# Performance work log

Measured on AMD Instinct MI355X. Metric: run time of the kernel, lower is better.

The kernel has to match this reference:

```python
import jax, jax.numpy as jnp
import numpy as np

DECAY = 0.9


def setup_inputs() -> dict:
    key = jax.random.key(0)
    k1, k2, k3 = jax.random.split(key, 3)
    B, S, D, M = 4, 4096, 1024, 4096
    x = jax.random.normal(k1, (B, S, D), dtype=jnp.float32)
    w1 = jax.random.normal(k2, (M, D), dtype=jnp.float32) * (1.0 / np.sqrt(D))
    w2 = jax.random.normal(k3, (D, M), dtype=jnp.float32) * (1.0 / np.sqrt(M))
    return {"x": x, "w1": w1, "w2": w2}


def reference(x, w1, w2):
    B, S, D = x.shape
    idx = jnp.arange(S)
    diff = idx[:, None] - idx[None, :]          # [S, S]
    mask = diff >= 0
    # clamp negative exponents before pow to avoid inf, then mask
    d = jnp.where(mask, diff, 0).astype(x.dtype)
    decay_matrix = (DECAY ** d) * (1.0 - DECAY) * mask.astype(x.dtype)  # [S, S]
    # causal exponential-decay EMA as dense matmul: current[b,t] = sum_s dm[t,s] x[b,s]
    current_states = jnp.einsum('ts,bsd->btd', decay_matrix, x)
    # roll by 1 with zeroed first step
    previous_states = jnp.concatenate(
        [jnp.zeros_like(current_states[:, :1]), current_states[:, :-1]], axis=1)
    # MemoryMLP: w2(silu(w1(prev)))
    h = jax.nn.silu(jnp.einsum('btd,md->btm', previous_states, w1))
    mem_out = jnp.einsum('btm,dm->btd', h, w2)
    final_state = current_states[:, -1, :]
    surprise_loss = jnp.mean((mem_out - jax.lax.stop_gradient(x)) ** 2)
    return mem_out, surprise_loss, final_state
```

## Files before the change

### kernel.cpp

```cpp
#include <hip/hip_runtime.h>
#include <hip/hip_bf16.h>
#include <stdint.h>

#define BSZ 4
#define SEQ 4096
#define DIM 1024
#define MDIM 4096
#define DECAYF 0.9f
#define OMD 0.1f
#define CHUNK 128
#define NCHUNK 32
#define DECAY_CHUNK 1.3901844577868923e-06f

typedef __bf16 bf16_t;
typedef __bf16 bf16x8 __attribute__((ext_vector_type(8)));
typedef __bf16 bf16x4 __attribute__((ext_vector_type(4)));
typedef float floatx4 __attribute__((ext_vector_type(4)));

__device__ __forceinline__ void load16_lds(const void* g, void* l) {
  __builtin_amdgcn_global_load_lds(
      (__attribute__((address_space(1))) void*)g,
      (__attribute__((address_space(3))) void*)l,
      16, 0, 0);
}

#define SB()  __builtin_amdgcn_sched_barrier(0)
#define BAR() __builtin_amdgcn_s_barrier()

__global__ void scan_chunk_kernel(const float* __restrict__ x,
                                  float* __restrict__ chunk_end) {
  int t = blockIdx.x * 256 + threadIdx.x;
  int d = t & (DIM - 1);
  int c = (t >> 10) & (NCHUNK - 1);
  int b = t >> 15;
  const float* xp = x + ((size_t)(b * SEQ + c * CHUNK + 64)) * DIM + d;
  float p = 0.f;
#pragma unroll 8
  for (int s = 0; s < 64; ++s) p = DECAYF * p + OMD * xp[(size_t)s * DIM];
  chunk_end[t] = p;
}

__global__ void scan_carry_kernel(const float* __restrict__ chunk_end,
                                  float* __restrict__ carry_in,
                                  float* __restrict__ final_state) {
  int t = blockIdx.x * 256 + threadIdx.x;
  int d = t & (DIM - 1);
  int b = t >> 10;
  float carry = 0.f;
#pragma unroll
  for (int c = 0; c < NCHUNK; ++c) {
    int idx = (b * NCHUNK + c) * DIM + d;
    carry_in[idx] = carry;
    carry = carry * DECAY_CHUNK + chunk_end[idx];
  }
  final_state[t] = carry;
}

__global__ void scan_emit_kernel(const float* __restrict__ x,
                                 const float* __restrict__ carry_in,
                                 bf16_t* __restrict__ prev) {
  int t = blockIdx.x * 256 + threadIdx.x;
  int d = t & (DIM - 1);
  int c = (t >> 10) & (NCHUNK - 1);
  int b = t >> 15;
  size_t base = ((size_t)(b * SEQ + c * CHUNK)) * DIM + d;
  const float* xp = x + base;
  bf16_t* pp = prev + base;
  float cs = carry_in[t];
#pragma unroll 4
  for (int s = 0; s < CHUNK; ++s) {
    pp[(size_t)s * DIM] = (bf16_t)cs;
    cs = DECAYF * cs + OMD * xp[(size_t)s * DIM];
  }
}

__global__ void cvt_bf16_kernel(const float* __restrict__ w, bf16_t* __restrict__ o) {
  int t = blockIdx.x * 256 + threadIdx.x;
  float4 v = ((const float4*)w)[t];
  bf16x4 r = { (bf16_t)v.x, (bf16_t)v.y, (bf16_t)v.z, (bf16_t)v.w };
  ((bf16x4*)o)[t] = r;
}

#define READ_A(dst, CA, MH)                                                    \
  _Pragma("unroll") for (int i_ = 0; i_ < 4; ++i_)                             \
      _Pragma("unroll") for (int k_ = 0; k_ < 2; ++k_)                         \
          dst[i_][k_] = *(const bf16x8*)((const char*)(CA) + wrBase +          \
                                         (MH) * 8192 + i_ * 2048 + rbase +     \
                                         ((k_ * 64 + kc) ^ lswz));

#define READ_B(dst, CB, NH)                                                    \
  _Pragma("unroll") for (int j_ = 0; j_ < 2; ++j_)                             \
      _Pragma("unroll") for (int k_ = 0; k_ < 2; ++k_)                         \
          dst[j_][k_] = *(const bf16x8*)((const char*)(CB) + wcBase +          \
                                         (NH) * 4096 + j_ * 2048 + rbase +     \
                                         ((k_ * 64 + kc) ^ lswz));

#define MMQ(AF, BF, MO, NO)                                                    \
  _Pragma("unroll") for (int k_ = 0; k_ < 2; ++k_)                             \
      _Pragma("unroll") for (int i_ = 0; i_ < 4; ++i_)                         \
          _Pragma("unroll") for (int j_ = 0; j_ < 2; ++j_)                     \
              acc[(MO) + i_][(NO) + j_] =                                      \
                  __builtin_amdgcn_mfma_f32_16x16x32_bf16(                     \
                      AF[i_][k_], BF[j_][k_], acc[(MO) + i_][(NO) + j_],       \
                      0, 0, 0);

template <int N, int K, int MT, int EPI>
__global__ __launch_bounds__(512, 1) void gemm256_kernel(
    const bf16_t* __restrict__ A, const bf16_t* __restrict__ B,
    void* __restrict__ Cout, const float* __restrict__ X,
    float* __restrict__ loss_acc) {
  constexpr int NT = N / 256;
  constexpr int NTK = K / 64;
  static_assert((NTK & 1) == 0 && NTK >= 4, "even K-tile count");
  static_assert(MT % 8 == 0, "m-tiles divisible by XCD count");
  __shared__ __attribute__((aligned(16))) bf16_t sA[2][16384];
  __shared__ __attribute__((aligned(16))) bf16_t sB[2][16384];

  const int tid = threadIdx.x;
  const int wave = tid >> 6;
  const int lane = tid & 63;
  const int bid = blockIdx.x;
  const int xcd = bid & 7;
  const int slot = bid >> 3;
  const int tm = (xcd * (MT / 8) + slot / NT) * 256;
  const int tn = (slot % NT) * 256;
  const int wr = wave >> 2;
  const int wc = wave & 3;
  const int wrBase = wr * 16384;
  const int wcBase = wc * 8192;
  const int rbase = (lane & 15) * 128;
  const int kc = (lane >> 4) * 16;
  const int lswz = ((lane >> 1) & 7) << 4;
  const int srow = wave * 8 + (lane >> 3);
  const int scolb = ((lane & 7) * 16) ^ (((srow >> 1) & 7) << 4);

  floatx4 acc[8][4];
#pragma unroll
  for (int i = 0; i < 8; ++i)
#pragma unroll
    for (int j = 0; j < 4; ++j) acc[i][j] = (floatx4){0.f, 0.f, 0.f, 0.f};

  bf16x8 a0[4][2], a1[4][2], b0[2][2], b1[2][2];

  auto stage_ht = [&](const bf16_t* G, int tb, bf16_t* lbuf, int kt, int h) {
    char* lbase = (char*)lbuf + h * 16384 + wave * 1024;
    const char* gbase =
        (const char*)G + ((size_t)(tb + h * 128 + srow) * K + kt) * 2 + scolb;
    load16_lds(gbase, lbase);
    load16_lds(gbase + (size_t)64 * K * 2, lbase + 8192);
  };

  auto tileQ = [&](int t, bf16_t* cA, bf16_t* cB, bf16_t* nA, bf16_t* nB) {
    const int kt2 = (t + 2) * 64;
    READ_B(b0, cB, 0);
    READ_B(b1, cB, 1);
    __builtin_amdgcn_s_setprio(1);
    MMQ(a0, b0, 0, 0);
    __builtin_amdgcn_s_setprio(0);
    BAR(); SB();
    READ_A(a1, cA, 1);
    __builtin_amdgcn_s_setprio(1);
    MMQ(a0, b1, 0, 2);
    __builtin_amdgcn_s_setprio(0);
    BAR(); SB();
    READ_B(b0, cB, 0);
    __builtin_amdgcn_s_setprio(1);
    MMQ(a1, b1, 4, 2);
    __builtin_amdgcn_s_setprio(0);
    if (t + 2 < NTK) {
      stage_ht(A, tm, cA, kt2, 0);
      stage_ht(A, tm, cA, kt2, 1);
      asm volatile("s_waitcnt vmcnt(4)");
    } else {
      asm volatile("s_waitcnt vmcnt(0)");
    }
    SB(); BAR(); SB();
    if (t + 1 < NTK) READ_A(a0, nA, 0);
    __builtin_amdgcn_s_setprio(1);
    MMQ(a1, b0, 4, 0);
    __builtin_amdgcn_s_setprio(0);
    if (t + 2 < NTK) {
      stage_ht(B, tn, cB, kt2, 0);
      stage_ht(B, tn, cB, kt2, 1);
    }
    BAR(); SB();
  };

  stage_ht(A, tm, sA[0], 0, 0);
  stage_ht(A, tm, sA[0], 0, 1);
  stage_ht(B, tn, sB[0], 0, 0);
  stage_ht(B, tn, sB[0], 0, 1);
  stage_ht(A, tm, sA[1], 64, 0);
  stage_ht(A, tm, sA[1], 64, 1);
  stage_ht(B, tn, sB[1], 64, 0);
  stage_ht(B, tn, sB[1], 64, 1);
  asm volatile("s_waitcnt vmcnt(8)");
  SB(); BAR(); SB();
  READ_A(a0, sA[0], 0);

#pragma unroll 1
  for (int t = 0; t < NTK; t += 2) {
    tileQ(t, sA[0], sB[0], sA[1], sB[1]);
    tileQ(t + 1, sA[1], sB[1], sA[0], sB[0]);
  }

  const int r0 = (lane >> 4) * 4;
  const int cn = lane & 15;
  if constexpr (EPI == 0) {
    bf16_t* H = (bf16_t*)Cout;
#pragma unroll
    for (int i = 0; i < 8; ++i)
#pragma unroll
      for (int j = 0; j < 4; ++j)
#pragma unroll
        for (int r = 0; r < 4; ++r) {
          int m = tm + wr * 128 + i * 16 + r0 + r;
          int n = tn + wc * 64 + j * 16 + cn;
          float v = acc[i][j][r];
          v = v / (1.f + __expf(-v));
          H[(size_t)m * N + n] = (bf16_t)v;
        }
  } else {
    float* O = (float*)Cout;
    float ls = 0.f;
#pragma unroll
    for (int i = 0; i < 8; ++i)
#pragma unroll
      for (int j = 0; j < 4; ++j)
#pragma unroll
        for (int r = 0; r < 4; ++r) {
          int m = tm + wr * 128 + i * 16 + r0 + r;
          int n = tn + wc * 64 + j * 16 + cn;
          size_t off = (size_t)m * N + n;
          float v = acc[i][j][r];
          O[off] = v;
          float dd = v - X[off];
          ls += dd * dd;
        }
#pragma unroll
    for (int s = 32; s > 0; s >>= 1) ls += __shfl_down(ls, s, 64);
    if (lane == 0) atomicAdd(loss_acc, ls);
  }
}

#undef READ_A
#undef READ_B
#undef MMQ

__global__ void finalize_loss_kernel(const float* __restrict__ loss_acc,
                                     float* __restrict__ out) {
  if (threadIdx.x == 0)
    out[0] = loss_acc[0] * (1.0f / (float)(BSZ * SEQ * DIM));
}

extern "C" void kernel_launch(void* const* d_in, const int* in_sizes, int n_in,
                              void* d_out, int out_size, void* d_ws, size_t ws_size,
                              hipStream_t stream) {
  const float* x  = (const float*)d_in[0];
  const float* w1 = (const float*)d_in[1];
  const float* w2 = (const float*)d_in[2];
  float* out = (float*)d_out;

  const int BT = BSZ * SEQ;
  char* ws = (char*)d_ws;
  bf16_t* prev      = (bf16_t*)(ws);
  bf16_t* h         = (bf16_t*)(ws + 33554432ull);
  bf16_t* w1b       = (bf16_t*)(ws + 167772160ull);
  bf16_t* w2b       = (bf16_t*)(ws + 176160768ull);
  float*  chunk_end = (float*)(ws + 184549376ull);
  float*  carry_in  = (float*)(ws + 185073664ull);
  float*  loss_acc  = (float*)(ws + 185597952ull);

  hipMemsetAsync(loss_acc, 0, sizeof(float), stream);

  cvt_bf16_kernel<<<4096, 256, 0, stream>>>(w1, w1b);
  cvt_bf16_kernel<<<4096, 256, 0, stream>>>(w2, w2b);

  scan_chunk_kernel<<<(BSZ * NCHUNK * DIM) / 256, 256, 0, stream>>>(x, chunk_end);
  scan_carry_kernel<<<(BSZ * DIM) / 256, 256, 0, stream>>>(chunk_end, carry_in,
                                                           out + 16777217);
  scan_emit_kernel<<<(BSZ * NCHUNK * DIM) / 256, 256, 0, stream>>>(x, carry_in, prev);

  gemm256_kernel<MDIM, DIM, BT / 256, 0>
      <<<(BT / 256) * (MDIM / 256), 512, 0, stream>>>(prev, w1b, h, nullptr, nullptr);

  gemm256_kernel<DIM, MDIM, BT / 256, 1>
      <<<(BT / 256) * (DIM / 256), 512, 0, stream>>>(h, w2b, out, x, loss_acc);

  finalize_loss_kernel<<<1, 64, 0, stream>>>(loss_acc, out + 16777216);
}
```

Before: 451.8 us.

## Restructure GEMM main loop prefetch schedule and merge weight conversion kernels

```diff
diff --git a/kernel.cpp b/kernel.cpp
--- a/kernel.cpp
+++ b/kernel.cpp
@@ -74,11 +74,17 @@
   }
 }
 
-__global__ void cvt_bf16_kernel(const float* __restrict__ w, bf16_t* __restrict__ o) {
-  int t = blockIdx.x * 256 + threadIdx.x;
-  float4 v = ((const float4*)w)[t];
+__global__ void cvt_bf16_kernel2(const float* __restrict__ wa,
+                                 bf16_t* __restrict__ oa,
+                                 const float* __restrict__ wb,
+                                 bf16_t* __restrict__ ob) {
+  int t = blockIdx.x * 256 + threadIdx.x;
+  const float* w = (t < 1048576) ? wa : wb;
+  bf16_t* o = (t < 1048576) ? oa : ob;
+  int i = t & 1048575;
+  float4 v = ((const float4*)w)[i];
   bf16x4 r = { (bf16_t)v.x, (bf16_t)v.y, (bf16_t)v.z, (bf16_t)v.w };
-  ((bf16x4*)o)[t] = r;
+  ((bf16x4*)o)[i] = r;
 }
 
 #define READ_A(dst, CA, MH)                                                    \
@@ -150,58 +156,58 @@
     load16_lds(gbase + (size_t)64 * K * 2, lbase + 8192);
   };
 
-  auto tileQ = [&](int t, bf16_t* cA, bf16_t* cB, bf16_t* nA, bf16_t* nB) {
-    const int kt2 = (t + 2) * 64;
+  auto tileT = [&](int t, bf16_t* cA, bf16_t* cB, bf16_t* nA, bf16_t* nB) {
+    const int kt1 = (t + 1) * 64;
+    const bool pf = (t + 1 < NTK);
+    READ_A(a0, cA, 0);
     READ_B(b0, cB, 0);
+    if (pf) { stage_ht(A, tm, nA, kt1, 0); stage_ht(B, tn, nB, kt1, 0); }
+    asm volatile("s_waitcnt lgkmcnt(8)"); SB();
+    BAR();
+    asm volatile("s_waitcnt lgkmcnt(0)"); SB();
+    __builtin_amdgcn_s_setprio(1);
+    MMQ(a0, b0, 0, 0);
+    __builtin_amdgcn_s_setprio(0);
+    if (pf) { asm volatile("s_waitcnt vmcnt(4)"); }
+    else    { asm volatile("s_waitcnt vmcnt(0)"); }
+    SB();
+    BAR(); SB();
     READ_B(b1, cB, 1);
-    __builtin_amdgcn_s_setprio(1);
-    MMQ(a0, b0, 0, 0);
+    if (pf) { stage_ht(A, tm, nA, kt1, 1); stage_ht(B, tn, nB, kt1, 1); }
+    BAR();
+    asm volatile("s_waitcnt lgkmcnt(0)"); SB();
+    __builtin_amdgcn_s_setprio(1);
+    MMQ(a0, b1, 0, 2);
     __builtin_amdgcn_s_setprio(0);
     BAR(); SB();
     READ_A(a1, cA, 1);
-    __builtin_amdgcn_s_setprio(1);
-    MMQ(a0, b1, 0, 2);
+    BAR();
+    asm volatile("s_waitcnt lgkmcnt(0)"); SB();
+    __builtin_amdgcn_s_setprio(1);
+    MMQ(a1, b1, 4, 2);
     __builtin_amdgcn_s_setprio(0);
     BAR(); SB();
     READ_B(b0, cB, 0);
-    __builtin_amdgcn_s_setprio(1);
-    MMQ(a1, b1, 4, 2);
-    __builtin_amdgcn_s_setprio(0);
-    if (t + 2 < NTK) {
-      stage_ht(A, tm, cA, kt2, 0);
-      stage_ht(A, tm, cA, kt2, 1);
-      asm volatile("s_waitcnt vmcnt(4)");
-    } else {
-      asm volatile("s_waitcnt vmcnt(0)");
-    }
-    SB(); BAR(); SB();
-    if (t + 1 < NTK) READ_A(a0, nA, 0);
+    BAR();
+    asm volatile("s_waitcnt lgkmcnt(0)"); SB();
     __builtin_amdgcn_s_setprio(1);
     MMQ(a1, b0, 4, 0);
     __builtin_amdgcn_s_setprio(0);
-    if (t + 2 < NTK) {
-      stage_ht(B, tn, cB, kt2, 0);
-      stage_ht(B, tn, cB, kt2, 1);
-    }
+    if (pf) { asm volatile("s_waitcnt vmcnt(4)"); SB(); }
     BAR(); SB();
   };
 
   stage_ht(A, tm, sA[0], 0, 0);
+  stage_ht(B, tn, sB[0], 0, 0);
   stage_ht(A, tm, sA[0], 0, 1);
-  stage_ht(B, tn, sB[0], 0, 0);
   stage_ht(B, tn, sB[0], 0, 1);
-  stage_ht(A, tm, sA[1], 64, 0);
-  stage_ht(A, tm, sA[1], 64, 1);
-  stage_ht(B, tn, sB[1], 64, 0);
-  stage_ht(B, tn, sB[1], 64, 1);
-  asm volatile("s_waitcnt vmcnt(8)");
+  asm volatile("s_waitcnt vmcnt(4)");
   SB(); BAR(); SB();
-  READ_A(a0, sA[0], 0);
 
 #pragma unroll 1
   for (int t = 0; t < NTK; t += 2) {
-    tileQ(t, sA[0], sB[0], sA[1], sB[1]);
-    tileQ(t + 1, sA[1], sB[1], sA[0], sB[0]);
+    tileT(t, sA[0], sB[0], sA[1], sB[1]);
+    tileT(t + 1, sA[1], sB[1], sA[0], sB[0]);
   }
 
   const int r0 = (lane >> 4) * 4;
@@ -273,8 +279,7 @@
 
   hipMemsetAsync(loss_acc, 0, sizeof(float), stream);
 
-  cvt_bf16_kernel<<<4096, 256, 0, stream>>>(w1, w1b);
-  cvt_bf16_kernel<<<4096, 256, 0, stream>>>(w2, w2b);
+  cvt_bf16_kernel2<<<8192, 256, 0, stream>>>(w1, w1b, w2, w2b);
 
   scan_chunk_kernel<<<(BSZ * NCHUNK * DIM) / 256, 256, 0, stream>>>(x, chunk_end);
   scan_carry_kernel<<<(BSZ * DIM) / 256, 256, 0, stream>>>(chunk_end, carry_in,
```

New measurement: 488.8 us. 1.08x slower.
